# Optimization experiments

Hardware: AMD Instinct MI355X
Metric: run time of the kernel (lower is better)

Reference implementation:

```python
import jax, jax.numpy as jnp
import numpy as np

B, S, E, C = 128, 256, 768, 4


def setup_inputs() -> dict:
    key = jax.random.key(0)
    ks = jax.random.split(key, 8)
    questions = jax.random.normal(ks[0], (B, E), dtype=jnp.float32)
    segments = jax.random.normal(ks[1], (B, S, E), dtype=jnp.float32)
    W1 = jax.random.normal(ks[2], (2 * E, E), dtype=jnp.float32) * 0.02
    b1 = jnp.zeros((E,), dtype=jnp.float32)
    W2 = jax.random.normal(ks[3], (E, E // 2), dtype=jnp.float32) * 0.02
    b2 = jnp.zeros((E // 2,), dtype=jnp.float32)
    W3 = jax.random.normal(ks[4], (E // 2, C), dtype=jnp.float32) * 0.02
    b3 = jnp.zeros((C,), dtype=jnp.float32)
    num_segments = jax.random.randint(ks[5], (B,), 1, S + 1, dtype=jnp.int32)
    return {"questions": questions, "segments": segments, "W1": W1, "b1": b1,
            "W2": W2, "b2": b2, "W3": W3, "b3": b3, "num_segments": num_segments}


def reference(questions, segments, W1, b1, W2, b2, W3, b3, num_segments):
    # --- MLP instance scores (call()): concat question emb with every segment emb ---
    q = jnp.broadcast_to(questions[:, None, :], segments.shape)      # [B,S,E]
    x = jnp.concatenate([q, segments], axis=-1)                      # [B,S,2E]
    h = jax.nn.gelu(x @ W1 + b1, approximate=False)                  # keras gelu is exact
    h = jax.nn.gelu(h @ W2 + b2, approximate=False)
    preds = jax.nn.softmax(h @ W3 + b3, axis=-1)                     # [B,S,C]

    # --- per-bag noisy-OR style aggregation (aggregate_loss inner math, vectorized) ---
    # In the TF code, for class cid: s_j = sum(preds[j,:cid]) (exclusive cumsum over
    # classes), and product_of_sum_prob ACCUMULATES across the i loop, so
    # update_i = preds[i,cid] * cumprod_i( prod_{j!=k} s_j ) (leave-one-out products).
    mask = jnp.arange(S)[None, :] < num_segments[:, None]            # [B,S]
    mC = mask[..., None]                                             # [B,S,1]
    s = jnp.cumsum(preds, axis=-1) - preds                           # exclusive cumsum, [B,S,C]
    s_m = jnp.where(mC, s, 1.0)                                      # padded -> multiplicative identity
    # leave-one-out product over the segment axis via prefix/suffix cumprods
    cp_f = jnp.cumprod(s_m, axis=1)
    prefix = jnp.concatenate([jnp.ones_like(s_m[:, :1]), cp_f[:, :-1]], axis=1)
    cp_b = jnp.cumprod(s_m[:, ::-1], axis=1)[:, ::-1]
    suffix = jnp.concatenate([cp_b[:, 1:], jnp.ones_like(s_m[:, :1])], axis=1)
    L = prefix * suffix                                              # prod_{j!=k} s_j, [B,S,C]
    cpL = jnp.cumprod(L, axis=1)                                     # running product over i (padding is at the end)
    sum_term = jnp.sum(jnp.where(mC, preds * cpL, 0.0), axis=1)      # [B,C]
    prod_term = jnp.prod(jnp.where(mC, preds, 1.0), axis=1)          # prod_i preds[i,cid]
    agg = sum_term / jnp.float32(C) + prod_term                      # bag_pred_agg_scores, [B,C]
    return agg
```

## Files before the change

kernel.cpp:

```cpp
#include <hip/hip_runtime.h>
#include <hip/hip_bf16.h>


typedef __attribute__((ext_vector_type(8))) short short8;
typedef __attribute__((ext_vector_type(8))) unsigned short ushort8;
typedef __attribute__((ext_vector_type(16))) float f32x16;
typedef __attribute__((ext_vector_type(8))) int i32x8;
typedef __attribute__((ext_vector_type(4))) int i32x4;

__device__ __forceinline__ unsigned short f2bf(float f) {
    union { float f; unsigned int u; } c; c.f = f;
    unsigned int u = c.u;
    unsigned int r = (u + 0x7FFFu + ((u >> 16) & 1u)) >> 16;
    return (unsigned short)r;
}
__device__ __forceinline__ float bf2f(unsigned short u) {
    union { unsigned int u; float f; } c; c.u = ((unsigned int)u) << 16;
    return c.f;
}
__device__ __forceinline__ float gelu_fast(float x) {
    float x2 = x * x;
    float y2 = 1.5957691216057308f * (x + 0.044715f * x2 * x);
    float e = __expf(y2);
    float t = 1.0f - 2.0f * __builtin_amdgcn_rcpf(e + 1.0f);
    return 0.5f * x * (1.0f + t);
}

typedef const __attribute__((address_space(1))) void* gas_t;
typedef __attribute__((address_space(3))) void* las_t;
__device__ __forceinline__ void g2l16(const void* g, void* l) {
    __builtin_amdgcn_global_load_lds((gas_t)g, (las_t)l, 16, 0, 0);
}

__device__ __forceinline__ unsigned int f4_to_fp8x4(float a, float b, float c, float d) {
    int lo = __builtin_amdgcn_cvt_pk_fp8_f32(a, b, 0, 0);
    return (unsigned int)__builtin_amdgcn_cvt_pk_fp8_f32(c, d, lo, 1);
}
__device__ __forceinline__ unsigned char f_to_fp8(float a) {
    return (unsigned char)(__builtin_amdgcn_cvt_pk_fp8_f32(a, a, 0, 0) & 0xFF);
}

#define PREP_Q    96
#define PREP_TR1E 240
#define PREP_TR2E 312
#define PREP_END  12600

__global__ __launch_bounds__(256) void prep_kernel(
    const float* __restrict__ segments, unsigned char* __restrict__ segF8,
    const float* __restrict__ W1, unsigned char* __restrict__ W1t8,
    const float* __restrict__ W2, unsigned char* __restrict__ W2t8,
    const float* __restrict__ questions, float* __restrict__ qW1p)
{
    __shared__ __align__(16) char sh[16640];
    const int bid = blockIdx.x, tid = threadIdx.x;

    if (bid < PREP_Q) {
        const int s = bid / 24, rem = bid % 24;
        const int n0 = (rem % 12) * 64, m0 = (rem / 12) * 64;
        float (*As)[64] = (float(*)[64])sh;
        float (*Bs)[64] = (float(*)[64])(sh + 4096);
        const int tn = tid & 15, tm = tid >> 4;
        float acc[4][4] = {};
        const int la_m = tid >> 2;
        const int la_k = (tid & 3) << 2;
        const int lb_k = tid >> 4;
        const int lb_n = (tid & 15) << 2;
        const float* Aptr = questions + (size_t)(m0 + la_m) * 768 + la_k;
        const float* Bptr = W1 + (size_t)lb_k * 768 + n0 + lb_n;
        const int kbeg = s * 192, kend = kbeg + 192;
        for (int k0 = kbeg; k0 < kend; k0 += 16) {
            float4 av = *(const float4*)(Aptr + k0);
            float4 bv = *(const float4*)(Bptr + (size_t)k0 * 768);
            As[la_k + 0][la_m] = av.x;
            As[la_k + 1][la_m] = av.y;
            As[la_k + 2][la_m] = av.z;
            As[la_k + 3][la_m] = av.w;
            *(float4*)&Bs[lb_k][lb_n] = bv;
            __syncthreads();
            #pragma unroll
            for (int k = 0; k < 16; k++) {
                float4 a = *(const float4*)&As[k][tm << 2];
                float4 b = *(const float4*)&Bs[k][tn << 2];
                float ar[4] = {a.x, a.y, a.z, a.w};
                float br[4] = {b.x, b.y, b.z, b.w};
                #pragma unroll
                for (int i = 0; i < 4; i++)
                    #pragma unroll
                    for (int j = 0; j < 4; j++)
                        acc[i][j] += ar[i] * br[j];
            }
            __syncthreads();
        }
        float* outp = qW1p + (size_t)s * 128 * 768;
        #pragma unroll
        for (int i = 0; i < 4; i++) {
            int row = m0 + (tm << 2) + i;
            int colBase = n0 + (tn << 2);
            *(float4*)&outp[(size_t)row * 768 + colBase] =
                make_float4(acc[i][0], acc[i][1], acc[i][2], acc[i][3]);
        }
        return;
    }

    if (bid < PREP_TR2E) {
        const float* in; unsigned char* outp; int R, C, bx, by;
        if (bid < PREP_TR1E) {
            int idx = bid - PREP_Q; bx = idx % 12; by = idx / 12;
            in = W1 + 768 * 768; outp = W1t8; R = 768; C = 768;
        } else {
            int idx = bid - PREP_TR1E; bx = idx % 6; by = idx / 6;
            in = W2; outp = W2t8; R = 768; C = 384;
        }
        float (*t)[65] = (float(*)[65])sh;
        int r0 = by * 64, c0 = bx * 64;
        int tx = tid & 63, ty = tid >> 6;
        #pragma unroll
        for (int p = 0; p < 16; p++) {
            int row = ty * 16 + p;
            t[row][tx] = in[(size_t)(r0 + row) * C + c0 + tx];
        }
        __syncthreads();
        #pragma unroll
        for (int p = 0; p < 16; p++) {
            int orow = ty * 16 + p;
            outp[(size_t)(c0 + orow) * R + r0 + tx] = f_to_fp8(t[tx][orow]);
        }
        return;
    }

    {
        long i = (long)(bid - PREP_TR2E) * 256 + tid;
        const float4* in = (const float4*)segments;
        float4 a = in[2 * i], b = in[2 * i + 1];
        unsigned int lo = f4_to_fp8x4(a.x, a.y, a.z, a.w);
        unsigned int hi = f4_to_fp8x4(b.x, b.y, b.z, b.w);
        *(uint2*)(segF8 + i * 8) = make_uint2(lo, hi);
    }
}

template<int OUT8>
__global__ __launch_bounds__(256) void mfma_gemm_f8(
    const unsigned char* __restrict__ A8,
    const unsigned char* __restrict__ Bt8,
    const float* __restrict__ bias,
    const float* __restrict__ rowAdd,
    void* __restrict__ CoutV,
    int M, int N, int K)
{
    __shared__ __align__(16) unsigned char smem8[32768];
    unsigned char* As = smem8;
    unsigned char* Bs = smem8 + 8192;
    const int tid = threadIdx.x;
    const int wave = tid >> 6, lane = tid & 63;
    const int m0 = blockIdx.y * 128, n0 = blockIdx.x * 128;
    const int wm = (wave & 1) * 64, wn = (wave >> 1) * 64;

    f32x16 acc[2][2] = {};

    const int srow = tid >> 2;
    const int schunk = (tid & 3) ^ ((srow >> 1) & 3);
    const unsigned char* Ag = A8 + (size_t)(m0 + srow) * K + schunk * 16;
    const unsigned char* Bg = Bt8 + (size_t)(n0 + srow) * K + schunk * 16;
    unsigned char* Al = As + tid * 16;
    unsigned char* Bl = Bs + tid * 16;

    const int fm = lane & 31, fq = lane >> 5;

    for (int k0 = 0; k0 < K; k0 += 64) {
        g2l16(Ag + k0, Al);
        g2l16(Ag + (size_t)64 * K + k0, Al + 4096);
        g2l16(Bg + k0, Bl);
        g2l16(Bg + (size_t)64 * K + k0, Bl + 4096);
        __syncthreads();

        i32x8 av[2], bv[2];
        #pragma unroll
        for (int i = 0; i < 2; i++) {
            int rw = wm + i * 32 + fm, key = (rw >> 1) & 3;
            i32x4 lo = *(const i32x4*)&As[rw * 64 + (((fq << 1) | 0) ^ key) * 16];
            i32x4 hi = *(const i32x4*)&As[rw * 64 + (((fq << 1) | 1) ^ key) * 16];
            av[i][0] = lo[0]; av[i][1] = lo[1]; av[i][2] = lo[2]; av[i][3] = lo[3];
            av[i][4] = hi[0]; av[i][5] = hi[1]; av[i][6] = hi[2]; av[i][7] = hi[3];
        }
        #pragma unroll
        for (int j = 0; j < 2; j++) {
            int rw = wn + j * 32 + fm, key = (rw >> 1) & 3;
            i32x4 lo = *(const i32x4*)&Bs[rw * 64 + (((fq << 1) | 0) ^ key) * 16];
            i32x4 hi = *(const i32x4*)&Bs[rw * 64 + (((fq << 1) | 1) ^ key) * 16];
            bv[j][0] = lo[0]; bv[j][1] = lo[1]; bv[j][2] = lo[2]; bv[j][3] = lo[3];
            bv[j][4] = hi[0]; bv[j][5] = hi[1]; bv[j][6] = hi[2]; bv[j][7] = hi[3];
        }
        #pragma unroll
        for (int i = 0; i < 2; i++)
            #pragma unroll
            for (int j = 0; j < 2; j++)
                acc[i][j] = __builtin_amdgcn_mfma_scale_f32_32x32x64_f8f6f4(
                    av[i], bv[j], acc[i][j], 0, 0,
                    0, 127, 0, 127);
        __syncthreads();
    }

    #pragma unroll
    for (int j = 0; j < 2; j++) {
        int coll = wn + j * 32 + fm;
        int col = n0 + coll;
        float add = bias[col];
        if (rowAdd) {
            const float* radd = rowAdd + (size_t)(m0 >> 8) * N;
            add += radd[col] + radd[col + 98304] +
                   radd[col + 2 * 98304] + radd[col + 3 * 98304];
        }
        #pragma unroll
        for (int i = 0; i < 2; i++) {
            int rbase = wm + i * 32 + 4 * fq;
            #pragma unroll
            for (int reg = 0; reg < 16; reg++) {
                int rowl = rbase + (reg & 3) + 8 * (reg >> 2);
                float v = gelu_fast(acc[i][j][reg] + add);
                if (OUT8) smem8[rowl * 128 + coll] = f_to_fp8(v);
                else ((unsigned short*)smem8)[rowl * 128 + coll] = f2bf(v);
            }
        }
    }
    __syncthreads();
    if (OUT8) {
        unsigned char* Cout = (unsigned char*)CoutV;
        #pragma unroll
        for (int it = 0; it < 4; it++) {
            int idx = it * 256 + tid;
            int r = idx >> 3, cc = (idx & 7) * 16;
            *(uint4*)&Cout[(size_t)(m0 + r) * N + n0 + cc] =
                *(const uint4*)&smem8[r * 128 + cc];
        }
    } else {
        unsigned short* Cout = (unsigned short*)CoutV;
        #pragma unroll
        for (int it = 0; it < 8; it++) {
            int idx = it * 256 + tid;
            int r = idx >> 4, cc = (idx & 15) * 8;
            *(ushort8*)&Cout[(size_t)(m0 + r) * N + n0 + cc] =
                *(const ushort8*)&((unsigned short*)smem8)[r * 128 + cc];
        }
    }
}

__device__ __forceinline__ float4 f4mul(float4 a, float4 b) {
    return make_float4(a.x * b.x, a.y * b.y, a.z * b.z, a.w * b.w);
}
__device__ float4 scan_prod(float4 v, float4* buf, int tid) {
    __syncthreads();
    buf[tid] = v;
    __syncthreads();
    #pragma unroll
    for (int off = 1; off < 256; off <<= 1) {
        float4 o = (tid >= off) ? buf[tid - off] : make_float4(1.f, 1.f, 1.f, 1.f);
        __syncthreads();
        v = f4mul(v, o);
        buf[tid] = v;
        __syncthreads();
    }
    return v;
}

__global__ __launch_bounds__(256) void head_kernel(
    const unsigned short* __restrict__ H2, const float* __restrict__ W3,
    const float* __restrict__ b3, const int* __restrict__ nseg,
    float* __restrict__ out)
{
    __shared__ float4 buf[256];
    __shared__ float4 w3s[384];
    const int b = blockIdx.x, tid = threadIdx.x;
    for (int i = tid; i < 384; i += 256) w3s[i] = ((const float4*)W3)[i];
    __syncthreads();

    const unsigned short* hrow = H2 + (size_t)(b * 256 + tid) * 384;
    float4 acc = make_float4(b3[0], b3[1], b3[2], b3[3]);
    #pragma unroll
    for (int kk = 0; kk < 48; kk++) {
        ushort8 u = *(const ushort8*)(hrow + kk * 8);
        #pragma unroll
        for (int j = 0; j < 8; j++) {
            float h = bf2f(u[j]);
            float4 w = w3s[kk * 8 + j];
            acc.x += h * w.x; acc.y += h * w.y; acc.z += h * w.z; acc.w += h * w.w;
        }
    }
    float m = fmaxf(fmaxf(acc.x, acc.y), fmaxf(acc.z, acc.w));
    float e0 = __expf(acc.x - m), e1 = __expf(acc.y - m),
          e2 = __expf(acc.z - m), e3 = __expf(acc.w - m);
    float inv = 1.0f / (e0 + e1 + e2 + e3);
    float4 p = make_float4(e0 * inv, e1 * inv, e2 * inv, e3 * inv);

    const int n = nseg[b];
    const float4 ones = make_float4(1.f, 1.f, 1.f, 1.f);
    bool msk = tid < n;
    float s1 = p.x, s2 = s1 + p.y, s3 = s2 + p.z;
    float4 sm = msk ? make_float4(0.f, s1, s2, s3) : ones;

    scan_prod(sm, buf, tid);
    float4 pfx = (tid > 0) ? buf[tid - 1] : ones;
    __syncthreads();

    buf[255 - tid] = sm;
    __syncthreads();
    float4 rsm = buf[tid];
    scan_prod(rsm, buf, tid);
    float4 sfx = (tid < 255) ? buf[254 - tid] : ones;

    float4 L = f4mul(pfx, sfx);
    float4 cpL = scan_prod(L, buf, tid);

    float4 term = msk ? f4mul(p, cpL) : make_float4(0.f, 0.f, 0.f, 0.f);
    float4 pm = msk ? p : ones;

    __syncthreads();
    buf[tid] = term;
    __syncthreads();
    for (int off = 128; off > 0; off >>= 1) {
        if (tid < off) {
            float4 a = buf[tid], c = buf[tid + off];
            buf[tid] = make_float4(a.x + c.x, a.y + c.y, a.z + c.z, a.w + c.w);
        }
        __syncthreads();
    }
    float4 sum_t = buf[0];
    __syncthreads();

    buf[tid] = pm;
    __syncthreads();
    for (int off = 128; off > 0; off >>= 1) {
        if (tid < off) buf[tid] = f4mul(buf[tid], buf[tid + off]);
        __syncthreads();
    }
    if (tid == 0) {
        float4 pr = buf[0];
        ((float4*)out)[b] = make_float4(0.25f * sum_t.x + pr.x,
                                        0.25f * sum_t.y + pr.y,
                                        0.25f * sum_t.z + pr.z,
                                        0.25f * sum_t.w + pr.w);
    }
}

extern "C" void kernel_launch(void* const* d_in, const int* in_sizes, int n_in,
                              void* d_out, int out_size, void* d_ws, size_t ws_size,
                              hipStream_t stream) {
    (void)in_sizes; (void)n_in; (void)out_size; (void)ws_size;
    const float* questions = (const float*)d_in[0];
    const float* segments  = (const float*)d_in[1];
    const float* W1 = (const float*)d_in[2];
    const float* b1 = (const float*)d_in[3];
    const float* W2 = (const float*)d_in[4];
    const float* b2 = (const float*)d_in[5];
    const float* W3 = (const float*)d_in[6];
    const float* b3 = (const float*)d_in[7];
    const int*  nseg = (const int*)d_in[8];
    float* out = (float*)d_out;

    char* w = (char*)d_ws;
    float* qW1p = (float*)w;                   w += (size_t)4 * 128 * 768 * 4;
    unsigned char*  W1t8 = (unsigned char*)w;  w += (size_t)768 * 768;
    unsigned char*  W2t8 = (unsigned char*)w;  w += (size_t)384 * 768;
    unsigned char*  segF8 = (unsigned char*)w; w += (size_t)32768 * 768;
    unsigned char*  H1f8 = (unsigned char*)w;  w += (size_t)32768 * 768;
    unsigned short* H2b  = (unsigned short*)w; w += (size_t)32768 * 384 * 2;

    prep_kernel<<<PREP_END, 256, 0, stream>>>(
        segments, segF8, W1, W1t8, W2, W2t8, questions, qW1p);
    mfma_gemm_f8<1><<<dim3(6, 256), 256, 0, stream>>>(
        segF8, W1t8, b1, qW1p, H1f8, 32768, 768, 768);
    mfma_gemm_f8<0><<<dim3(3, 256), 256, 0, stream>>>(
        H1f8, W2t8, b2, nullptr, H2b, 32768, 384, 768);
    head_kernel<<<128, 256, 0, stream>>>(H2b, W3, b3, nseg, out);
}
```

Measured before the change: 245.8 us.

## Fuse W3 projection into second GEMM epilogue and deepen K tile to 128

The second GEMM now computes the 4-class logits directly in its epilogue. It multiplies the bf16 GELU tile by a W3 slice held in LDS and atomically accumulates partial logits. This removes the 32768x384 bf16 H2 write and its re-read in the head kernel, at the cost of atomics and a memset. Both GEMMs also stage K=128 per iteration with an 8-chunk XOR swizzle, which halves the barrier count per K.

```diff
diff --git a/kernel.cpp b/kernel.cpp
--- a/kernel.cpp
+++ b/kernel.cpp
@@ -138,18 +138,28 @@
     }
 }
 
-template<int OUT8>
-__global__ __launch_bounds__(256) void mfma_gemm_f8(
+__device__ __forceinline__ i32x8 frag_f8(const unsigned char* base, int row, int s, int fq) {
+    const int key = row & 7;
+    const int c0 = s * 4 + fq * 2;
+    i32x4 lo = *(const i32x4*)&base[row * 128 + ((c0 + 0) ^ key) * 16];
+    i32x4 hi = *(const i32x4*)&base[row * 128 + ((c0 + 1) ^ key) * 16];
+    i32x8 v;
+    v[0] = lo[0]; v[1] = lo[1]; v[2] = lo[2]; v[3] = lo[3];
+    v[4] = hi[0]; v[5] = hi[1]; v[6] = hi[2]; v[7] = hi[3];
+    return v;
+}
+
+__global__ __launch_bounds__(256) void k2_f8(
     const unsigned char* __restrict__ A8,
     const unsigned char* __restrict__ Bt8,
     const float* __restrict__ bias,
     const float* __restrict__ rowAdd,
-    void* __restrict__ CoutV,
+    unsigned char* __restrict__ Cout,
     int M, int N, int K)
 {
     __shared__ __align__(16) unsigned char smem8[32768];
     unsigned char* As = smem8;
-    unsigned char* Bs = smem8 + 8192;
+    unsigned char* Bs = smem8 + 16384;
     const int tid = threadIdx.x;
     const int wave = tid >> 6, lane = tid & 63;
     const int m0 = blockIdx.y * 128, n0 = blockIdx.x * 128;
@@ -157,8 +167,8 @@
 
     f32x16 acc[2][2] = {};
 
-    const int srow = tid >> 2;
-    const int schunk = (tid & 3) ^ ((srow >> 1) & 3);
+    const int srow = tid >> 3;
+    const int schunk = (tid & 7) ^ (srow & 7);
     const unsigned char* Ag = A8 + (size_t)(m0 + srow) * K + schunk * 16;
     const unsigned char* Bg = Bt8 + (size_t)(n0 + srow) * K + schunk * 16;
     unsigned char* Al = As + tid * 16;
@@ -166,81 +176,141 @@
 
     const int fm = lane & 31, fq = lane >> 5;
 
-    for (int k0 = 0; k0 < K; k0 += 64) {
-        g2l16(Ag + k0, Al);
-        g2l16(Ag + (size_t)64 * K + k0, Al + 4096);
-        g2l16(Bg + k0, Bl);
-        g2l16(Bg + (size_t)64 * K + k0, Bl + 4096);
-        __syncthreads();
-
-        i32x8 av[2], bv[2];
-        #pragma unroll
-        for (int i = 0; i < 2; i++) {
-            int rw = wm + i * 32 + fm, key = (rw >> 1) & 3;
-            i32x4 lo = *(const i32x4*)&As[rw * 64 + (((fq << 1) | 0) ^ key) * 16];
-            i32x4 hi = *(const i32x4*)&As[rw * 64 + (((fq << 1) | 1) ^ key) * 16];
-            av[i][0] = lo[0]; av[i][1] = lo[1]; av[i][2] = lo[2]; av[i][3] = lo[3];
-            av[i][4] = hi[0]; av[i][5] = hi[1]; av[i][6] = hi[2]; av[i][7] = hi[3];
-        }
-        #pragma unroll
-        for (int j = 0; j < 2; j++) {
-            int rw = wn + j * 32 + fm, key = (rw >> 1) & 3;
-            i32x4 lo = *(const i32x4*)&Bs[rw * 64 + (((fq << 1) | 0) ^ key) * 16];
-            i32x4 hi = *(const i32x4*)&Bs[rw * 64 + (((fq << 1) | 1) ^ key) * 16];
-            bv[j][0] = lo[0]; bv[j][1] = lo[1]; bv[j][2] = lo[2]; bv[j][3] = lo[3];
-            bv[j][4] = hi[0]; bv[j][5] = hi[1]; bv[j][6] = hi[2]; bv[j][7] = hi[3];
-        }
-        #pragma unroll
-        for (int i = 0; i < 2; i++)
-            #pragma unroll
-            for (int j = 0; j < 2; j++)
-                acc[i][j] = __builtin_amdgcn_mfma_scale_f32_32x32x64_f8f6f4(
-                    av[i], bv[j], acc[i][j], 0, 0,
-                    0, 127, 0, 127);
-        __syncthreads();
-    }
-
+    for (int k0 = 0; k0 < K; k0 += 128) {
+        #pragma unroll
+        for (int r = 0; r < 4; r++) {
+            g2l16(Ag + k0 + (size_t)(32 * r) * K, Al + r * 4096);
+            g2l16(Bg + k0 + (size_t)(32 * r) * K, Bl + r * 4096);
+        }
+        __syncthreads();
+
+        #pragma unroll
+        for (int s = 0; s < 2; s++) {
+            i32x8 av[2], bv[2];
+            #pragma unroll
+            for (int i = 0; i < 2; i++) av[i] = frag_f8(As, wm + i * 32 + fm, s, fq);
+            #pragma unroll
+            for (int j = 0; j < 2; j++) bv[j] = frag_f8(Bs, wn + j * 32 + fm, s, fq);
+            #pragma unroll
+            for (int i = 0; i < 2; i++)
+                #pragma unroll
+                for (int j = 0; j < 2; j++)
+                    acc[i][j] = __builtin_amdgcn_mfma_scale_f32_32x32x64_f8f6f4(
+                        av[i], bv[j], acc[i][j], 0, 0, 0, 127, 0, 127);
+        }
+        __syncthreads();
+    }
+
+    const float* radd = rowAdd + (size_t)(m0 >> 8) * N;
     #pragma unroll
     for (int j = 0; j < 2; j++) {
         int coll = wn + j * 32 + fm;
         int col = n0 + coll;
-        float add = bias[col];
-        if (rowAdd) {
-            const float* radd = rowAdd + (size_t)(m0 >> 8) * N;
-            add += radd[col] + radd[col + 98304] +
-                   radd[col + 2 * 98304] + radd[col + 3 * 98304];
-        }
+        float add = bias[col] + radd[col] + radd[col + 98304] +
+                    radd[col + 2 * 98304] + radd[col + 3 * 98304];
         #pragma unroll
         for (int i = 0; i < 2; i++) {
             int rbase = wm + i * 32 + 4 * fq;
             #pragma unroll
             for (int reg = 0; reg < 16; reg++) {
                 int rowl = rbase + (reg & 3) + 8 * (reg >> 2);
-                float v = gelu_fast(acc[i][j][reg] + add);
-                if (OUT8) smem8[rowl * 128 + coll] = f_to_fp8(v);
-                else ((unsigned short*)smem8)[rowl * 128 + coll] = f2bf(v);
+                smem8[rowl * 128 + coll] = f_to_fp8(gelu_fast(acc[i][j][reg] + add));
             }
         }
     }
     __syncthreads();
-    if (OUT8) {
-        unsigned char* Cout = (unsigned char*)CoutV;
-        #pragma unroll
-        for (int it = 0; it < 4; it++) {
-            int idx = it * 256 + tid;
-            int r = idx >> 3, cc = (idx & 7) * 16;
-            *(uint4*)&Cout[(size_t)(m0 + r) * N + n0 + cc] =
-                *(const uint4*)&smem8[r * 128 + cc];
-        }
-    } else {
-        unsigned short* Cout = (unsigned short*)CoutV;
-        #pragma unroll
-        for (int it = 0; it < 8; it++) {
-            int idx = it * 256 + tid;
-            int r = idx >> 4, cc = (idx & 15) * 8;
-            *(ushort8*)&Cout[(size_t)(m0 + r) * N + n0 + cc] =
-                *(const ushort8*)&((unsigned short*)smem8)[r * 128 + cc];
-        }
+    #pragma unroll
+    for (int it = 0; it < 4; it++) {
+        int idx = it * 256 + tid;
+        int r = idx >> 3, cc = (idx & 7) * 16;
+        *(uint4*)&Cout[(size_t)(m0 + r) * N + n0 + cc] =
+            *(const uint4*)&smem8[r * 128 + cc];
+    }
+}
+
+__global__ __launch_bounds__(256) void k3_f8_logits(
+    const unsigned char* __restrict__ A8,
+    const unsigned char* __restrict__ Bt8,
+    const float* __restrict__ bias,
+    const float* __restrict__ W3,
+    float* __restrict__ logits,
+    int M, int N, int K)
+{
+    __shared__ __align__(16) unsigned char smem8[32768 + 2048];
+    unsigned char* As = smem8;
+    unsigned char* Bs = smem8 + 16384;
+    unsigned short* cst = (unsigned short*)smem8;
+    float4* w3l = (float4*)(smem8 + 32768);
+    const int tid = threadIdx.x;
+    const int wave = tid >> 6, lane = tid & 63;
+    const int m0 = blockIdx.y * 128, n0 = blockIdx.x * 128;
+    const int wm = (wave & 1) * 64, wn = (wave >> 1) * 64;
+
+    f32x16 acc[2][2] = {};
+
+    const int srow = tid >> 3;
+    const int schunk = (tid & 7) ^ (srow & 7);
+    const unsigned char* Ag = A8 + (size_t)(m0 + srow) * K + schunk * 16;
+    const unsigned char* Bg = Bt8 + (size_t)(n0 + srow) * K + schunk * 16;
+    unsigned char* Al = As + tid * 16;
+    unsigned char* Bl = Bs + tid * 16;
+
+    const int fm = lane & 31, fq = lane >> 5;
+
+    for (int k0 = 0; k0 < K; k0 += 128) {
+        #pragma unroll
+        for (int r = 0; r < 4; r++) {
+            g2l16(Ag + k0 + (size_t)(32 * r) * K, Al + r * 4096);
+            g2l16(Bg + k0 + (size_t)(32 * r) * K, Bl + r * 4096);
+        }
+        __syncthreads();
+
+        #pragma unroll
+        for (int s = 0; s < 2; s++) {
+            i32x8 av[2], bv[2];
+            #pragma unroll
+            for (int i = 0; i < 2; i++) av[i] = frag_f8(As, wm + i * 32 + fm, s, fq);
+            #pragma unroll
+            for (int j = 0; j < 2; j++) bv[j] = frag_f8(Bs, wn + j * 32 + fm, s, fq);
+            #pragma unroll
+            for (int i = 0; i < 2; i++)
+                #pragma unroll
+                for (int j = 0; j < 2; j++)
+                    acc[i][j] = __builtin_amdgcn_mfma_scale_f32_32x32x64_f8f6f4(
+                        av[i], bv[j], acc[i][j], 0, 0, 0, 127, 0, 127);
+        }
+        __syncthreads();
+    }
+
+    #pragma unroll
+    for (int j = 0; j < 2; j++) {
+        int coll = wn + j * 32 + fm;
+        float add = bias[n0 + coll];
+        #pragma unroll
+        for (int i = 0; i < 2; i++) {
+            int rbase = wm + i * 32 + 4 * fq;
+            #pragma unroll
+            for (int reg = 0; reg < 16; reg++) {
+                int rowl = rbase + (reg & 3) + 8 * (reg >> 2);
+                cst[rowl * 128 + coll] = f2bf(gelu_fast(acc[i][j][reg] + add));
+            }
+        }
+    }
+    if (tid < 128) w3l[tid] = ((const float4*)W3)[n0 + tid];
+    __syncthreads();
+
+    #pragma unroll
+    for (int it = 0; it < 2; it++) {
+        int idx = it * 256 + tid;
+        int r = idx >> 2, c = idx & 3;
+        float sum = 0.f;
+        #pragma unroll 8
+        for (int cc = 0; cc < 128; cc++) {
+            float4 w = w3l[cc];
+            float wc = (c == 0) ? w.x : (c == 1) ? w.y : (c == 2) ? w.z : w.w;
+            sum += bf2f(cst[r * 128 + cc]) * wc;
+        }
+        atomicAdd(&logits[(size_t)(m0 + r) * 4 + c], sum);
     }
 }
 
@@ -263,31 +333,17 @@
 }
 
 __global__ __launch_bounds__(256) void head_kernel(
-    const unsigned short* __restrict__ H2, const float* __restrict__ W3,
-    const float* __restrict__ b3, const int* __restrict__ nseg,
-    float* __restrict__ out)
+    const float* __restrict__ logits, const float* __restrict__ b3,
+    const int* __restrict__ nseg, float* __restrict__ out)
 {
     __shared__ float4 buf[256];
-    __shared__ float4 w3s[384];
     const int b = blockIdx.x, tid = threadIdx.x;
-    for (int i = tid; i < 384; i += 256) w3s[i] = ((const float4*)W3)[i];
-    __syncthreads();
-
-    const unsigned short* hrow = H2 + (size_t)(b * 256 + tid) * 384;
-    float4 acc = make_float4(b3[0], b3[1], b3[2], b3[3]);
-    #pragma unroll
-    for (int kk = 0; kk < 48; kk++) {
-        ushort8 u = *(const ushort8*)(hrow + kk * 8);
-        #pragma unroll
-        for (int j = 0; j < 8; j++) {
-            float h = bf2f(u[j]);
-            float4 w = w3s[kk * 8 + j];
-            acc.x += h * w.x; acc.y += h * w.y; acc.z += h * w.z; acc.w += h * w.w;
-        }
-    }
-    float m = fmaxf(fmaxf(acc.x, acc.y), fmaxf(acc.z, acc.w));
-    float e0 = __expf(acc.x - m), e1 = __expf(acc.y - m),
-          e2 = __expf(acc.z - m), e3 = __expf(acc.w - m);
+
+    float4 z = ((const float4*)logits)[b * 256 + tid];
+    z.x += b3[0]; z.y += b3[1]; z.z += b3[2]; z.w += b3[3];
+    float m = fmaxf(fmaxf(z.x, z.y), fmaxf(z.z, z.w));
+    float e0 = __expf(z.x - m), e1 = __expf(z.y - m),
+          e2 = __expf(z.z - m), e3 = __expf(z.w - m);
     float inv = 1.0f / (e0 + e1 + e2 + e3);
     float4 p = make_float4(e0 * inv, e1 * inv, e2 * inv, e3 * inv);
 
@@ -362,13 +418,14 @@
     unsigned char*  W2t8 = (unsigned char*)w;  w += (size_t)384 * 768;
     unsigned char*  segF8 = (unsigned char*)w; w += (size_t)32768 * 768;
     unsigned char*  H1f8 = (unsigned char*)w;  w += (size_t)32768 * 768;
-    unsigned short* H2b  = (unsigned short*)w; w += (size_t)32768 * 384 * 2;
-
+    float* logits = (float*)w;                 w += (size_t)32768 * 4 * 4;
+
+    hipMemsetAsync(logits, 0, (size_t)32768 * 4 * 4, stream);
     prep_kernel<<<PREP_END, 256, 0, stream>>>(
         segments, segF8, W1, W1t8, W2, W2t8, questions, qW1p);
-    mfma_gemm_f8<1><<<dim3(6, 256), 256, 0, stream>>>(
+    k2_f8<<<dim3(6, 256), 256, 0, stream>>>(
         segF8, W1t8, b1, qW1p, H1f8, 32768, 768, 768);
-    mfma_gemm_f8<0><<<dim3(3, 256), 256, 0, stream>>>(
-        H1f8, W2t8, b2, nullptr, H2b, 32768, 384, 768);
-    head_kernel<<<128, 256, 0, stream>>>(H2b, W3, b3, nseg, out);
-}
+    k3_f8_logits<<<dim3(3, 256), 256, 0, stream>>>(
+        H1f8, W2t8, b2, W3, logits, 32768, 384, 768);
+    head_kernel<<<128, 256, 0, stream>>>(logits, b3, nseg, out);
+}
```

Result: slower. 266.7 us (+8.5%).
